# Kernel tuning notes

Measured on AMD Instinct MI355X. Metric: run time of the kernel, lower is better.

Reference implementation:

```python
import jax, jax.numpy as jnp
import numpy as np

B, S, D = 4, 2048, 1024
ATTN_D, OUT_D, H = 1024, 1024, 16
EPS = 1e-12


def setup_inputs() -> dict:
    key = jax.random.key(0)
    ks = jax.random.split(key, 9)
    s = 0.02
    return {
        "x": jax.random.normal(ks[0], (B, S, D), dtype=jnp.float32),
        "wq": jax.random.normal(ks[1], (D, ATTN_D), dtype=jnp.float32) * s,
        "bq": jnp.zeros((ATTN_D,), dtype=jnp.float32),
        "wk": jax.random.normal(ks[2], (D, ATTN_D), dtype=jnp.float32) * s,
        "bk": jnp.zeros((ATTN_D,), dtype=jnp.float32),
        "wv": jax.random.normal(ks[3], (D, ATTN_D), dtype=jnp.float32) * s,
        "bv": jnp.zeros((ATTN_D,), dtype=jnp.float32),
        "wo": jax.random.normal(ks[4], (ATTN_D, OUT_D), dtype=jnp.float32) * s,
        "bo": jnp.zeros((OUT_D,), dtype=jnp.float32),
        "ln_g": jnp.ones((OUT_D,), dtype=jnp.float32),
        "ln_b": jnp.zeros((OUT_D,), dtype=jnp.float32),
    }


def reference(x, wq, bq, wk, bk, wv, bv, wo, bo, ln_g, ln_b):
    b, s, _ = x.shape
    hd = ATTN_D // H  # head_dim
    # projections -> [B, H, S, hd]
    q = (x @ wq + bq).reshape(b, s, H, hd).transpose(0, 2, 1, 3)
    k = (x @ wk + bk).reshape(b, s, H, hd).transpose(0, 2, 1, 3)
    v = (x @ wv + bv).reshape(b, s, H, hd).transpose(0, 2, 1, 3)
    # full O(S^2) score matrix, as in the original module
    scores = jnp.einsum("bhqd,bhkd->bhqk", q, k) / jnp.sqrt(jnp.float32(hd))
    attn = jax.nn.softmax(scores, axis=-1)
    out = jnp.einsum("bhqk,bhkd->bhqd", attn, v)
    out = out.transpose(0, 2, 1, 3).reshape(b, s, ATTN_D)
    out = out @ wo + bo
    # LayerNorm (no residual in this module)
    mu = jnp.mean(out, axis=-1, keepdims=True)
    var = jnp.var(out, axis=-1, keepdims=True)
    out = (out - mu) * jax.lax.rsqrt(var + EPS) * ln_g + ln_b
    return out
```

## Files before the change

### kernel.cpp

```cpp
#include <hip/hip_runtime.h>

typedef __bf16 bf16;
typedef __bf16 bf16x4 __attribute__((ext_vector_type(4)));
typedef __bf16 bf16x8 __attribute__((ext_vector_type(8)));
typedef float f32x4 __attribute__((ext_vector_type(4)));

#define NB 4
#define NS 2048
#define ND 1024
#define NH 16
#define HD 64

#define QSCALE 0.18033688f

__device__ __forceinline__ void gload_lds16(const void* g, void* l) {
  __builtin_amdgcn_global_load_lds(
      (const __attribute__((address_space(1))) void*)g,
      (__attribute__((address_space(3))) void*)l, 16, 0, 0);
}

__device__ __forceinline__ float fast_exp2(float x) {
#if __has_builtin(__builtin_amdgcn_exp2f)
  return __builtin_amdgcn_exp2f(x);
#else
  return exp2f(x);
#endif
}

__global__ __launch_bounds__(256) void k_cvt(const float* __restrict__ src,
                                             bf16* __restrict__ dst) {
  size_t i = ((size_t)blockIdx.x * 256 + threadIdx.x) * 4;
  float4 v = *(const float4*)(src + i);
  bf16x4 o = {(__bf16)v.x, (__bf16)v.y, (__bf16)v.z, (__bf16)v.w};
  *(bf16x4*)(dst + i) = o;
}

__global__ __launch_bounds__(256) void k_cvt_T4(const float* __restrict__ wq,
                                                const float* __restrict__ wk,
                                                const float* __restrict__ wv,
                                                const float* __restrict__ wo,
                                                bf16* __restrict__ wqkvT,
                                                bf16* __restrict__ woT) {
  int z = blockIdx.z;
  const float* src = z == 0 ? wq : z == 1 ? wk : z == 2 ? wv : wo;
  bf16* dst = z < 3 ? wqkvT + (size_t)z * 1048576 : woT;
  __shared__ float t[32][33];
  int tx = threadIdx.x, ty = threadIdx.y;
  int x = blockIdx.x * 32 + tx;
  int y = blockIdx.y * 32 + ty;
#pragma unroll
  for (int j = 0; j < 4; ++j)
    t[ty + j * 8][tx] = src[(size_t)(y + j * 8) * 1024 + x];
  __syncthreads();
  int x2 = blockIdx.y * 32 + tx;
  int y2 = blockIdx.x * 32 + ty;
#pragma unroll
  for (int j = 0; j < 4; ++j)
    dst[(size_t)(y2 + j * 8) * 1024 + x2] = (__bf16)t[tx][ty + j * 8];
}

__global__ __launch_bounds__(256) void k_vT(const bf16* __restrict__ V,
                                            bf16* __restrict__ Vt) {
  __shared__ bf16 t[64][72];
  int tid = threadIdx.x;
  int bh = blockIdx.x >> 5, st = blockIdx.x & 31;
  int b = bh >> 4, h = bh & 15;
  const bf16* src = V + ((size_t)b * NS + st * 64) * ND + h * HD;
#pragma unroll
  for (int rep = 0; rep < 2; ++rep) {
    int idx = rep * 256 + tid;
    int r = idx >> 3, c8 = (idx & 7) * 8;
    *(bf16x8*)&t[r][c8] = *(const bf16x8*)(src + (size_t)r * ND + c8);
  }
  __syncthreads();
  bf16* dst = Vt + (size_t)bh * HD * NS + st * 64;
#pragma unroll
  for (int rep = 0; rep < 2; ++rep) {
    int idx = rep * 256 + tid;
    int d = idx >> 3, s8 = (idx & 7) * 8;
    bf16x8 v;
#pragma unroll
    for (int j = 0; j < 8; ++j) {
      int jj = (j + tid) & 7;
      v[jj] = t[s8 + jj][d];
    }
    *(bf16x8*)(dst + (size_t)d * NS + s8) = v;
  }
}

__device__ __forceinline__ void gemm256_mainloop(const bf16* __restrict__ A,
                                                 const bf16* __restrict__ BT,
                                                 int bm, int bn, bf16* As,
                                                 bf16* Bs, f32x4 acc[4][4]) {
  const int tid = threadIdx.x;
  const int w = tid >> 6, lane = tid & 63, quad = lane >> 4, l15 = lane & 15;
  const int l7 = l15 & 7, l8 = lane >> 3;
  const int wr = w >> 1, wc = w & 1;
  const int gsw = ((lane & 7) ^ l8) * 8;
  const bf16* gaw = A + (size_t)(bm * 256 + w * 8 + l8) * 1024 + gsw;
  const bf16* gbw = BT + (size_t)(bn * 128 + w * 8 + l8) * 1024 + gsw;
  bf16* daw = As + w * 512;
  bf16* dbw = Bs + w * 512;
  int aoff[4][2], boff[4][2];
#pragma unroll
  for (int mi = 0; mi < 4; ++mi)
#pragma unroll
    for (int ks = 0; ks < 2; ++ks)
      aoff[mi][ks] =
          (wr * 64 + mi * 16 + l15) * 64 + (((ks * 4 + quad) ^ l7) * 8);
#pragma unroll
  for (int ni = 0; ni < 4; ++ni)
#pragma unroll
    for (int ks = 0; ks < 2; ++ks)
      boff[ni][ks] =
          (wc * 64 + ni * 16 + l15) * 64 + (((ks * 4 + quad) ^ l7) * 8);

#pragma unroll
  for (int ri = 0; ri < 4; ++ri)
    gload_lds16(gaw + (size_t)(ri * 64) * 1024, daw + ri * 4096);
#pragma unroll
  for (int ri = 0; ri < 2; ++ri)
    gload_lds16(gbw + (size_t)(ri * 64) * 1024, dbw + ri * 4096);

  for (int kt = 0; kt < 16; ++kt) {
    const int buf = kt & 1;
    __syncthreads();
    if (kt + 1 < 16) {
      const bf16* ga = gaw + (kt + 1) * 64;
      const bf16* gb = gbw + (kt + 1) * 64;
      bf16* da = daw + (buf ^ 1) * 16384;
      bf16* db = dbw + (buf ^ 1) * 8192;
#pragma unroll
      for (int ri = 0; ri < 4; ++ri)
        gload_lds16(ga + (size_t)(ri * 64) * 1024, da + ri * 4096);
#pragma unroll
      for (int ri = 0; ri < 2; ++ri)
        gload_lds16(gb + (size_t)(ri * 64) * 1024, db + ri * 4096);
    }
    const bf16* a_ = As + buf * 16384;
    const bf16* b_ = Bs + buf * 8192;
#pragma unroll
    for (int ks = 0; ks < 2; ++ks) {
      bf16x8 av[4], bv[4];
#pragma unroll
      for (int i = 0; i < 4; ++i)
        av[i] = *(const bf16x8*)(a_ + aoff[i][ks]);
#pragma unroll
      for (int i = 0; i < 4; ++i)
        bv[i] = *(const bf16x8*)(b_ + boff[i][ks]);
#pragma unroll
      for (int mi = 0; mi < 4; ++mi)
#pragma unroll
        for (int ni = 0; ni < 4; ++ni)
          acc[mi][ni] = __builtin_amdgcn_mfma_f32_16x16x32_bf16(
              av[mi], bv[ni], acc[mi][ni], 0, 0, 0);
    }
  }
  __syncthreads();
}

__global__ __launch_bounds__(512, 2) void k_gemm_qkv(
    const bf16* __restrict__ A, const bf16* __restrict__ BT,
    const float* __restrict__ bq, const float* __restrict__ bk,
    const float* __restrict__ bv, bf16* __restrict__ Q, bf16* __restrict__ K,
    bf16* __restrict__ V) {
  __shared__ alignas(16) char smem[98304];
  bf16* As = (bf16*)smem;
  bf16* Bs = (bf16*)(smem + 65536);
  f32x4 acc[4][4] = {};
  const int bm = blockIdx.y, bn = blockIdx.x;
  gemm256_mainloop(A, BT, bm, bn, As, Bs, acc);
  const int tid = threadIdx.x;
  const int w = tid >> 6, lane = tid & 63, quad = lane >> 4, l15 = lane & 15;
  const int wr = w >> 1, wc = w & 1;
  bf16* sEw = (bf16*)smem + w * 4608;
  const int colbase = bn * 128 + wc * 64;
  const int which = colbase >> 10;
  const int nnbase = colbase & 1023;
  const float* bias = which == 0 ? bq : which == 1 ? bk : bv;
  bf16* dst = which == 0 ? Q : which == 1 ? K : V;
  const float scl = which == 0 ? QSCALE : 1.f;
  const int rowbase = bm * 256 + wr * 64;
#pragma unroll
  for (int ni = 0; ni < 4; ++ni) {
    float bb = bias[nnbase + ni * 16 + l15];
#pragma unroll
    for (int mi = 0; mi < 4; ++mi)
#pragma unroll
      for (int r = 0; r < 4; ++r)
        sEw[(mi * 16 + quad * 4 + r) * 72 + ni * 16 + l15] =
            (__bf16)((acc[mi][ni][r] + bb) * scl);
  }
  const int l8 = lane >> 3, g8 = (lane & 7) * 8;
#pragma unroll
  for (int i = 0; i < 8; ++i) {
    int row = i * 8 + l8;
    bf16x8 vv = *(const bf16x8*)(sEw + row * 72 + g8);
    *(bf16x8*)(dst + (size_t)(rowbase + row) * 1024 + nnbase + g8) = vv;
  }
}

__global__ __launch_bounds__(512, 2) void k_gemm_out(const bf16* __restrict__ A,
                                                     const bf16* __restrict__ BT,
                                                     const float* __restrict__ bo,
                                                     float* __restrict__ Y) {
  __shared__ alignas(16) char smem[98304];
  bf16* As = (bf16*)smem;
  bf16* Bs = (bf16*)(smem + 65536);
  f32x4 acc[4][4] = {};
  const int bm = blockIdx.y, bn = blockIdx.x;
  gemm256_mainloop(A, BT, bm, bn, As, Bs, acc);
  const int tid = threadIdx.x;
  const int w = tid >> 6, lane = tid & 63, quad = lane >> 4, l15 = lane & 15;
  const int wr = w >> 1, wc = w & 1;
  float* sEw = (float*)smem + w * 2176;
  const int colbase = bn * 128 + wc * 64;
  const int rowbase = bm * 256 + wr * 64;
  float bb[4];
#pragma unroll
  for (int ni = 0; ni < 4; ++ni) bb[ni] = bo[colbase + ni * 16 + l15];
  const int l4 = lane >> 4, c4 = (lane & 15) * 4;
#pragma unroll
  for (int h2 = 0; h2 < 2; ++h2) {
#pragma unroll
    for (int ml = 0; ml < 2; ++ml)
#pragma unroll
      for (int ni = 0; ni < 4; ++ni)
#pragma unroll
        for (int r = 0; r < 4; ++r)
          sEw[(ml * 16 + quad * 4 + r) * 68 + ni * 16 + l15] =
              acc[h2 * 2 + ml][ni][r] + bb[ni];
#pragma unroll
    for (int i = 0; i < 8; ++i) {
      int row = i * 4 + l4;
      float4 v = *(const float4*)(sEw + row * 68 + c4);
      *(float4*)(Y + (size_t)(rowbase + h2 * 32 + row) * 1024 + colbase + c4) =
          v;
    }
  }
}

__global__ __launch_bounds__(256, 4) void k_attn(const bf16* __restrict__ Qg,
                                                 const bf16* __restrict__ Kg,
                                                 const bf16* __restrict__ VtG,
                                                 bf16* __restrict__ O) {
  __shared__ alignas(16) char smem[40960];
  bf16* sK = (bf16*)smem;
  bf16* sVt = (bf16*)(smem + 16384);
  const int tid = threadIdx.x;
  const int w = tid >> 6, lane = tid & 63, quad = lane >> 4, l15 = lane & 15;
  const int l7 = l15 & 7, l8 = lane >> 3;
  const int sw = (l15 >> 1) & 3;
  const int bh = blockIdx.x & 63;
  const int qt = blockIdx.x >> 6;
  const int b = bh >> 4, h = bh & 15;
  const bf16* Qh = Qg + (size_t)b * NS * ND + h * HD;
  const bf16* Kh = Kg + (size_t)b * NS * ND + h * HD;
  const bf16* Vh = VtG + (size_t)bh * HD * NS;
  bf16* Pw = (bf16*)(smem + 32768) + w * 1024;

  const int q0 = qt * 128 + w * 32;
  bf16x8 qb[2][2];
#pragma unroll
  for (int ni = 0; ni < 2; ++ni)
#pragma unroll
    for (int ks = 0; ks < 2; ++ks)
      qb[ni][ks] = *(const bf16x8*)(Qh + (size_t)(q0 + ni * 16 + l15) * ND +
                                    ks * 32 + quad * 8);

  const int gsw = ((lane & 7) ^ l8) * 8;
  const bf16* gk = Kh + (size_t)(w * 8 + l8) * ND + gsw;
  const bf16* gv = Vh + (size_t)(w * 8 + l8) * NS + gsw;
  bf16* dk = sK + w * 512;
  bf16* dv = sVt + w * 512;

  f32x4 o_acc[4][2] = {};
  float l_run[2] = {0.f, 0.f};

  int offA[4][2];
#pragma unroll
  for (int mi = 0; mi < 4; ++mi)
#pragma unroll
    for (int ks = 0; ks < 2; ++ks)
      offA[mi][ks] = (mi * 16 + l15) * 64 + (((ks * 4 + quad) ^ l7) * 8);
  int offP[2], wbase[2], wg[2];
#pragma unroll
  for (int ni = 0; ni < 2; ++ni) {
    offP[ni] = (ni * 16 + l15) * 32 + ((quad ^ sw) * 8);
    wbase[ni] = (ni * 16 + l15) * 32 + (quad & 1) * 4;
  }
#pragma unroll
  for (int m2 = 0; m2 < 2; ++m2)
    wg[m2] = (((m2 * 2 + (quad >> 1)) ^ sw) * 8);

  gload_lds16(gk, dk);
  gload_lds16(gk + 32 * ND, dk + 2048);
  gload_lds16(gv, dv);
  gload_lds16(gv + 32 * NS, dv + 2048);

  for (int it = 0; it < NS / 64; ++it) {
    const int buf = (it & 1) * 4096;
    __syncthreads();
    if (it + 1 < NS / 64) {
      const int nbuf = 4096 - buf;
      const bf16* gk1 = gk + (size_t)(it + 1) * 64 * ND;
      const bf16* gv1 = gv + (it + 1) * 64;
      gload_lds16(gk1, dk + nbuf);
      gload_lds16(gk1 + 32 * ND, dk + nbuf + 2048);
      gload_lds16(gv1, dv + nbuf);
      gload_lds16(gv1 + 32 * NS, dv + nbuf + 2048);
    }

#pragma unroll
    for (int hf = 0; hf < 2; ++hf) {
#pragma unroll
      for (int m2 = 0; m2 < 2; ++m2) {
        const int mi = 2 * hf + m2;
        f32x4 s[2] = {};
#pragma unroll
        for (int ks = 0; ks < 2; ++ks) {
          bf16x8 ak = *(const bf16x8*)(sK + buf + offA[mi][ks]);
#pragma unroll
          for (int ni = 0; ni < 2; ++ni)
            s[ni] = __builtin_amdgcn_mfma_f32_16x16x32_bf16(ak, qb[ni][ks],
                                                            s[ni], 0, 0, 0);
        }
#pragma unroll
        for (int ni = 0; ni < 2; ++ni) {
#pragma unroll
          for (int r = 0; r < 4; ++r) {
            s[ni][r] = fast_exp2(s[ni][r]);
            l_run[ni] += s[ni][r];
          }
          bf16x4 p = {(__bf16)s[ni][0], (__bf16)s[ni][1], (__bf16)s[ni][2],
                      (__bf16)s[ni][3]};
          *(bf16x4*)(Pw + wbase[ni] + wg[m2]) = p;
        }
      }

      bf16x8 pb[2];
#pragma unroll
      for (int ni = 0; ni < 2; ++ni)
        pb[ni] = *(const bf16x8*)(Pw + offP[ni]);
#pragma unroll
      for (int mi = 0; mi < 4; ++mi) {
        bf16x8 av = *(const bf16x8*)(sVt + buf + offA[mi][hf]);
#pragma unroll
        for (int ni = 0; ni < 2; ++ni)
          o_acc[mi][ni] = __builtin_amdgcn_mfma_f32_16x16x32_bf16(
              av, pb[ni], o_acc[mi][ni], 0, 0, 0);
      }
    }
  }

#pragma unroll
  for (int ni = 0; ni < 2; ++ni) {
    float l = l_run[ni];
    l += __shfl_xor(l, 16, 64);
    l += __shfl_xor(l, 32, 64);
    float inv = 1.f / l;
    int q = q0 + ni * 16 + l15;
    size_t orow = ((size_t)b * NS + q) * 1024 + h * 64;
#pragma unroll
    for (int mi = 0; mi < 4; ++mi) {
      bf16x4 ov = {
          (__bf16)(o_acc[mi][ni][0] * inv), (__bf16)(o_acc[mi][ni][1] * inv),
          (__bf16)(o_acc[mi][ni][2] * inv), (__bf16)(o_acc[mi][ni][3] * inv)};
      *(bf16x4*)(O + orow + mi * 16 + quad * 4) = ov;
    }
  }
}

__global__ __launch_bounds__(256) void k_ln(float* __restrict__ Y,
                                            const float* __restrict__ g,
                                            const float* __restrict__ bta) {
  int row = blockIdx.x, tid = threadIdx.x;
  float4 v = ((const float4*)(Y + (size_t)row * 1024))[tid];
  float sm = v.x + v.y + v.z + v.w;
  float sq = v.x * v.x + v.y * v.y + v.z * v.z + v.w * v.w;
#pragma unroll
  for (int off = 1; off < 64; off <<= 1) {
    sm += __shfl_xor(sm, off, 64);
    sq += __shfl_xor(sq, off, 64);
  }
  __shared__ float red[8];
  int w = tid >> 6, lane = tid & 63;
  if (lane == 0) {
    red[w] = sm;
    red[4 + w] = sq;
  }
  __syncthreads();
  sm = red[0] + red[1] + red[2] + red[3];
  sq = red[4] + red[5] + red[6] + red[7];
  float mu = sm * (1.f / 1024.f);
  float var = sq * (1.f / 1024.f) - mu * mu;
  float rstd = rsqrtf(var + 1e-12f);
  float4 g4 = ((const float4*)g)[tid];
  float4 b4 = ((const float4*)bta)[tid];
  float4 o;
  o.x = (v.x - mu) * rstd * g4.x + b4.x;
  o.y = (v.y - mu) * rstd * g4.y + b4.y;
  o.z = (v.z - mu) * rstd * g4.z + b4.z;
  o.w = (v.w - mu) * rstd * g4.w + b4.w;
  ((float4*)(Y + (size_t)row * 1024))[tid] = o;
}

extern "C" void kernel_launch(void* const* d_in, const int* in_sizes, int n_in,
                              void* d_out, int out_size, void* d_ws,
                              size_t ws_size, hipStream_t stream) {
  const float* x = (const float*)d_in[0];
  const float* wq = (const float*)d_in[1];
  const float* bq = (const float*)d_in[2];
  const float* wk = (const float*)d_in[3];
  const float* bk = (const float*)d_in[4];
  const float* wv = (const float*)d_in[5];
  const float* bv = (const float*)d_in[6];
  const float* wo = (const float*)d_in[7];
  const float* bo = (const float*)d_in[8];
  const float* ln_g = (const float*)d_in[9];
  const float* ln_b = (const float*)d_in[10];
  float* out = (float*)d_out;

  char* ws = (char*)d_ws;
  bf16* xb = (bf16*)ws;          ws += 16777216;
  bf16* wqkvT = (bf16*)ws;       ws += 6291456;
  bf16* woT = (bf16*)ws;         ws += 2097152;
  bf16* Qh = (bf16*)ws;          ws += 16777216;
  bf16* Kh = (bf16*)ws;          ws += 16777216;
  bf16* Vh = (bf16*)ws;          ws += 16777216;
  bf16* Vt = (bf16*)ws;          ws += 16777216;
  bf16* AOb = (bf16*)ws;         ws += 16777216;

  k_cvt<<<8192, 256, 0, stream>>>(x, xb);
  dim3 tb(32, 8);
  k_cvt_T4<<<dim3(32, 32, 4), tb, 0, stream>>>(wq, wk, wv, wo, wqkvT, woT);

  k_gemm_qkv<<<dim3(24, 32), 512, 0, stream>>>(xb, wqkvT, bq, bk, bv, Qh, Kh,
                                               Vh);
  k_vT<<<NB * NH * 32, 256, 0, stream>>>(Vh, Vt);
  k_attn<<<NB * NH * (NS / 128), 256, 0, stream>>>(Qh, Kh, Vt, AOb);
  k_gemm_out<<<dim3(8, 32), 512, 0, stream>>>(AOb, woT, bo, out);
  k_ln<<<8192, 256, 0, stream>>>(out, ln_g, ln_b);
}
```

Before: 289.8 us.

## Triple-buffer GEMM mainloop with vmcnt waits, split LDS reads, and MFMA priority

Changes the shared GEMM mainloop from double to triple buffering. Global-to-LDS loads are issued two K-tiles ahead, and the loop waits with explicit s_waitcnt vmcnt plus a raw barrier, so only one barrier is needed per iteration. It also splits the A-fragment LDS reads into two halves interleaved with the MFMA groups and raises wave priority around the MFMAs. LDS per block grows from 96KB to 144KB, which at the declared launch bound of 2 blocks of 512 threads per CU may exceed LDS capacity and reduce occupancy to one block.

```diff
diff --git a/kernel.cpp b/kernel.cpp
--- a/kernel.cpp
+++ b/kernel.cpp
@@ -115,46 +115,72 @@
       boff[ni][ks] =
           (wc * 64 + ni * 16 + l15) * 64 + (((ks * 4 + quad) ^ l7) * 8);
 
-#pragma unroll
-  for (int ri = 0; ri < 4; ++ri)
-    gload_lds16(gaw + (size_t)(ri * 64) * 1024, daw + ri * 4096);
-#pragma unroll
-  for (int ri = 0; ri < 2; ++ri)
-    gload_lds16(gbw + (size_t)(ri * 64) * 1024, dbw + ri * 4096);
+  auto stage = [&](int kt) {
+    const int slot = kt % 3;
+    const bf16* ga = gaw + kt * 64;
+    const bf16* gb = gbw + kt * 64;
+    bf16* da = daw + slot * 16384;
+    bf16* db = dbw + slot * 8192;
+#pragma unroll
+    for (int ri = 0; ri < 4; ++ri)
+      gload_lds16(ga + (size_t)(ri * 64) * 1024, da + ri * 4096);
+#pragma unroll
+    for (int ri = 0; ri < 2; ++ri)
+      gload_lds16(gb + (size_t)(ri * 64) * 1024, db + ri * 4096);
+  };
+
+  stage(0);
+  stage(1);
+  asm volatile("s_waitcnt vmcnt(6)" ::: "memory");
+  __builtin_amdgcn_s_barrier();
 
   for (int kt = 0; kt < 16; ++kt) {
-    const int buf = kt & 1;
-    __syncthreads();
-    if (kt + 1 < 16) {
-      const bf16* ga = gaw + (kt + 1) * 64;
-      const bf16* gb = gbw + (kt + 1) * 64;
-      bf16* da = daw + (buf ^ 1) * 16384;
-      bf16* db = dbw + (buf ^ 1) * 8192;
-#pragma unroll
-      for (int ri = 0; ri < 4; ++ri)
-        gload_lds16(ga + (size_t)(ri * 64) * 1024, da + ri * 4096);
-#pragma unroll
-      for (int ri = 0; ri < 2; ++ri)
-        gload_lds16(gb + (size_t)(ri * 64) * 1024, db + ri * 4096);
-    }
-    const bf16* a_ = As + buf * 16384;
-    const bf16* b_ = Bs + buf * 8192;
-#pragma unroll
-    for (int ks = 0; ks < 2; ++ks) {
-      bf16x8 av[4], bv[4];
-#pragma unroll
-      for (int i = 0; i < 4; ++i)
-        av[i] = *(const bf16x8*)(a_ + aoff[i][ks]);
-#pragma unroll
-      for (int i = 0; i < 4; ++i)
-        bv[i] = *(const bf16x8*)(b_ + boff[i][ks]);
-#pragma unroll
-      for (int mi = 0; mi < 4; ++mi)
-#pragma unroll
-        for (int ni = 0; ni < 4; ++ni)
+    const int slot = kt % 3;
+    if (kt + 2 < 16) stage(kt + 2);
+    const bf16* a_ = As + slot * 16384;
+    const bf16* b_ = Bs + slot * 8192;
+    bf16x8 av[2][2], bv[4][2];
+#pragma unroll
+    for (int mi = 0; mi < 2; ++mi)
+#pragma unroll
+      for (int ks = 0; ks < 2; ++ks)
+        av[mi][ks] = *(const bf16x8*)(a_ + aoff[mi][ks]);
+#pragma unroll
+    for (int ni = 0; ni < 4; ++ni)
+#pragma unroll
+      for (int ks = 0; ks < 2; ++ks)
+        bv[ni][ks] = *(const bf16x8*)(b_ + boff[ni][ks]);
+    __builtin_amdgcn_s_setprio(1);
+#pragma unroll
+    for (int mi = 0; mi < 2; ++mi)
+#pragma unroll
+      for (int ni = 0; ni < 4; ++ni)
+#pragma unroll
+        for (int ks = 0; ks < 2; ++ks)
           acc[mi][ni] = __builtin_amdgcn_mfma_f32_16x16x32_bf16(
-              av[mi], bv[ni], acc[mi][ni], 0, 0, 0);
-    }
+              av[mi][ks], bv[ni][ks], acc[mi][ni], 0, 0, 0);
+    __builtin_amdgcn_s_setprio(0);
+    bf16x8 av2[2][2];
+#pragma unroll
+    for (int mi = 0; mi < 2; ++mi)
+#pragma unroll
+      for (int ks = 0; ks < 2; ++ks)
+        av2[mi][ks] = *(const bf16x8*)(a_ + aoff[2 + mi][ks]);
+    __builtin_amdgcn_s_setprio(1);
+#pragma unroll
+    for (int mi = 0; mi < 2; ++mi)
+#pragma unroll
+      for (int ni = 0; ni < 4; ++ni)
+#pragma unroll
+        for (int ks = 0; ks < 2; ++ks)
+          acc[2 + mi][ni] = __builtin_amdgcn_mfma_f32_16x16x32_bf16(
+              av2[mi][ks], bv[ni][ks], acc[2 + mi][ni], 0, 0, 0);
+    __builtin_amdgcn_s_setprio(0);
+    if (kt + 2 < 16)
+      asm volatile("s_waitcnt vmcnt(6)" ::: "memory");
+    else
+      asm volatile("s_waitcnt vmcnt(0)" ::: "memory");
+    if (kt + 1 < 16) __builtin_amdgcn_s_barrier();
   }
   __syncthreads();
 }
@@ -164,9 +190,9 @@
     const float* __restrict__ bq, const float* __restrict__ bk,
     const float* __restrict__ bv, bf16* __restrict__ Q, bf16* __restrict__ K,
     bf16* __restrict__ V) {
-  __shared__ alignas(16) char smem[98304];
+  __shared__ alignas(16) char smem[147456];
   bf16* As = (bf16*)smem;
-  bf16* Bs = (bf16*)(smem + 65536);
+  bf16* Bs = (bf16*)(smem + 98304);
   f32x4 acc[4][4] = {};
   const int bm = blockIdx.y, bn = blockIdx.x;
   gemm256_mainloop(A, BT, bm, bn, As, Bs, acc);
@@ -204,9 +230,9 @@
                                                      const bf16* __restrict__ BT,
                                                      const float* __restrict__ bo,
                                                      float* __restrict__ Y) {
-  __shared__ alignas(16) char smem[98304];
+  __shared__ alignas(16) char smem[147456];
   bf16* As = (bf16*)smem;
-  bf16* Bs = (bf16*)(smem + 65536);
+  bf16* Bs = (bf16*)(smem + 98304);
   f32x4 acc[4][4] = {};
   const int bm = blockIdx.y, bn = blockIdx.x;
   gemm256_mainloop(A, BT, bm, bn, As, Bs, acc);
```

Result: slower. 297.4 us (+2.6%).

## Halve GEMM K-tile to 32 and raise launch-bounds occupancy to 4

Applied to the files above, without the earlier changes.

The GEMM mainloop now stages K-slices of 32 instead of 64, with a new XOR swizzle and a single-pass MFMA loop. This shrinks staging LDS and lets the shared buffer drop to 72 KB. Launch bounds request 4 blocks per CU to increase occupancy. The costs are twice as many barrier iterations and a tighter register budget that may spill, while the LDS size may still cap residency below the requested level.

```diff
diff --git a/kernel.cpp b/kernel.cpp
--- a/kernel.cpp
+++ b/kernel.cpp
@@ -94,79 +94,61 @@
                                                  bf16* Bs, f32x4 acc[4][4]) {
   const int tid = threadIdx.x;
   const int w = tid >> 6, lane = tid & 63, quad = lane >> 4, l15 = lane & 15;
-  const int l7 = l15 & 7, l8 = lane >> 3;
   const int wr = w >> 1, wc = w & 1;
-  const int gsw = ((lane & 7) ^ l8) * 8;
-  const bf16* gaw = A + (size_t)(bm * 256 + w * 8 + l8) * 1024 + gsw;
-  const bf16* gbw = BT + (size_t)(bn * 128 + w * 8 + l8) * 1024 + gsw;
-  bf16* daw = As + w * 512;
-  bf16* dbw = Bs + w * 512;
-  int aoff[4][2], boff[4][2];
+  const int sw = (l15 >> 1) & 3;
+  const int r4 = tid >> 2, g4 = tid & 3;
+  const int gswz = (g4 ^ ((r4 >> 1) & 3)) * 8;
+  const bf16* gA = A + (size_t)(bm * 256 + r4) * 1024 + gswz;
+  const bf16* gB = BT + (size_t)(bn * 128 + r4) * 1024 + gswz;
+  bf16* dA = As + w * 512;
+  bf16* dB = Bs + w * 512;
+  int aoff[4], boff[4];
 #pragma unroll
   for (int mi = 0; mi < 4; ++mi)
-#pragma unroll
-    for (int ks = 0; ks < 2; ++ks)
-      aoff[mi][ks] =
-          (wr * 64 + mi * 16 + l15) * 64 + (((ks * 4 + quad) ^ l7) * 8);
+    aoff[mi] = (wr * 64 + mi * 16 + l15) * 32 + ((quad ^ sw) * 8);
 #pragma unroll
   for (int ni = 0; ni < 4; ++ni)
-#pragma unroll
-    for (int ks = 0; ks < 2; ++ks)
-      boff[ni][ks] =
-          (wc * 64 + ni * 16 + l15) * 64 + (((ks * 4 + quad) ^ l7) * 8);
-
-#pragma unroll
-  for (int ri = 0; ri < 4; ++ri)
-    gload_lds16(gaw + (size_t)(ri * 64) * 1024, daw + ri * 4096);
-#pragma unroll
-  for (int ri = 0; ri < 2; ++ri)
-    gload_lds16(gbw + (size_t)(ri * 64) * 1024, dbw + ri * 4096);
-
-  for (int kt = 0; kt < 16; ++kt) {
+    boff[ni] = (wc * 64 + ni * 16 + l15) * 32 + ((quad ^ sw) * 8);
+
+  auto stage = [&](int kt, int slot) {
+    const bf16* ga = gA + kt * 32;
+    const bf16* gb = gB + kt * 32;
+    gload_lds16(ga, dA + slot * 8192);
+    gload_lds16(ga + (size_t)128 * 1024, dA + slot * 8192 + 4096);
+    gload_lds16(gb, dB + slot * 4096);
+  };
+
+  stage(0, 0);
+  for (int kt = 0; kt < 32; ++kt) {
     const int buf = kt & 1;
     __syncthreads();
-    if (kt + 1 < 16) {
-      const bf16* ga = gaw + (kt + 1) * 64;
-      const bf16* gb = gbw + (kt + 1) * 64;
-      bf16* da = daw + (buf ^ 1) * 16384;
-      bf16* db = dbw + (buf ^ 1) * 8192;
-#pragma unroll
-      for (int ri = 0; ri < 4; ++ri)
-        gload_lds16(ga + (size_t)(ri * 64) * 1024, da + ri * 4096);
-#pragma unroll
-      for (int ri = 0; ri < 2; ++ri)
-        gload_lds16(gb + (size_t)(ri * 64) * 1024, db + ri * 4096);
-    }
-    const bf16* a_ = As + buf * 16384;
-    const bf16* b_ = Bs + buf * 8192;
-#pragma unroll
-    for (int ks = 0; ks < 2; ++ks) {
-      bf16x8 av[4], bv[4];
-#pragma unroll
-      for (int i = 0; i < 4; ++i)
-        av[i] = *(const bf16x8*)(a_ + aoff[i][ks]);
-#pragma unroll
-      for (int i = 0; i < 4; ++i)
-        bv[i] = *(const bf16x8*)(b_ + boff[i][ks]);
-#pragma unroll
-      for (int mi = 0; mi < 4; ++mi)
-#pragma unroll
-        for (int ni = 0; ni < 4; ++ni)
-          acc[mi][ni] = __builtin_amdgcn_mfma_f32_16x16x32_bf16(
-              av[mi], bv[ni], acc[mi][ni], 0, 0, 0);
+    if (kt + 1 < 32) stage(kt + 1, buf ^ 1);
+    const bf16* a_ = As + buf * 8192;
+    const bf16* b_ = Bs + buf * 4096;
+    bf16x8 bv[4];
+#pragma unroll
+    for (int ni = 0; ni < 4; ++ni) bv[ni] = *(const bf16x8*)(b_ + boff[ni]);
+#pragma unroll
+    for (int mi = 0; mi < 4; ++mi) {
+      bf16x8 av = *(const bf16x8*)(a_ + aoff[mi]);
+#pragma unroll
+      for (int ni = 0; ni < 4; ++ni)
+        acc[mi][ni] = __builtin_amdgcn_mfma_f32_16x16x32_bf16(av, bv[ni],
+                                                              acc[mi][ni], 0,
+                                                              0, 0);
     }
   }
   __syncthreads();
 }
 
-__global__ __launch_bounds__(512, 2) void k_gemm_qkv(
+__global__ __launch_bounds__(512, 4) void k_gemm_qkv(
     const bf16* __restrict__ A, const bf16* __restrict__ BT,
     const float* __restrict__ bq, const float* __restrict__ bk,
     const float* __restrict__ bv, bf16* __restrict__ Q, bf16* __restrict__ K,
     bf16* __restrict__ V) {
-  __shared__ alignas(16) char smem[98304];
+  __shared__ alignas(16) char smem[73728];
   bf16* As = (bf16*)smem;
-  bf16* Bs = (bf16*)(smem + 65536);
+  bf16* Bs = (bf16*)(smem + 32768);
   f32x4 acc[4][4] = {};
   const int bm = blockIdx.y, bn = blockIdx.x;
   gemm256_mainloop(A, BT, bm, bn, As, Bs, acc);
@@ -200,13 +182,12 @@
   }
 }
 
-__global__ __launch_bounds__(512, 2) void k_gemm_out(const bf16* __restrict__ A,
-                                                     const bf16* __restrict__ BT,
-                                                     const float* __restrict__ bo,
-                                                     float* __restrict__ Y) {
-  __shared__ alignas(16) char smem[98304];
+__global__ __launch_bounds__(512, 4) void k_gemm_out(
+    const bf16* __restrict__ A, const bf16* __restrict__ BT,
+    const float* __restrict__ bo, float* __restrict__ Y) {
+  __shared__ alignas(16) char smem[73728];
   bf16* As = (bf16*)smem;
-  bf16* Bs = (bf16*)(smem + 65536);
+  bf16* Bs = (bf16*)(smem + 32768);
   f32x4 acc[4][4] = {};
   const int bm = blockIdx.y, bn = blockIdx.x;
   gemm256_mainloop(A, BT, bm, bn, As, Bs, acc);
```

Result: no change. 294.4 us (+1.6%).
